# Kernel tuning notes

Hardware: AMD Instinct MI355X
Metric: run time of the kernel (lower is better)

The kernel has to match this reference:

```python
import jax, jax.numpy as jnp
import numpy as np
from jax import lax

N = 256
BATCH = 4096
N_MZIS = N * (N - 1) // 2  # 32640


def _reck_positions(n):
    # Static MZI position schedule: for layer in range(n-1): for pos in range(n-1-layer)
    return np.concatenate([np.arange(n - 1 - layer) for layer in range(n - 1)]).astype(np.int32)


def setup_inputs() -> dict:
    key = jax.random.key(0)
    k1, k2, k3, k4 = jax.random.split(key, 4)
    x = jax.random.normal(k1, (BATCH, N), dtype=jnp.float32)
    theta = jax.random.uniform(k2, (N_MZIS,), dtype=jnp.float32) * (np.pi / 2)
    phi_internal = jax.random.uniform(k3, (N_MZIS,), dtype=jnp.float32) * (2 * np.pi)
    phi_external = jax.random.uniform(k4, (N,), dtype=jnp.float32) * (2 * np.pi)
    return {"x": x, "theta": theta, "phi_internal": phi_internal, "phi_external": phi_external}


def _construct_unitary(theta, phi_internal, phi_external):
    n = phi_external.shape[0]
    positions = jnp.asarray(_reck_positions(n))  # [n_mzis], static schedule

    def step(U, inputs):
        pos, th, ph = inputs
        # Extract the two rows touched by this MZI and apply the 2x2 transfer matrix:
        # [[cos,          -sin*e^{-i phi}],
        #  [sin*e^{i phi}, cos          ]]
        rows = lax.dynamic_slice(U, (pos, jnp.int32(0)), (2, n))  # [2, n]
        r0, r1 = rows[0], rows[1]
        c = jnp.cos(th)
        s = jnp.sin(th)
        e = jnp.cos(ph) + 1j * jnp.sin(ph)
        new_rows = jnp.stack([c * r0 - s * jnp.conj(e) * r1,
                              s * e * r0 + c * r1])
        return lax.dynamic_update_slice(U, new_rows, (pos, jnp.int32(0))), None

    U0 = jnp.eye(n, dtype=jnp.complex64)
    U, _ = lax.scan(step, U0, (positions, theta, phi_internal))
    # Final external phase screen: diag(e^{i phi_ext}) @ U
    phase = jnp.cos(phi_external) + 1j * jnp.sin(phi_external)
    return phase[:, None] * U


def reference(x, theta, phi_internal, phi_external):
    U = _construct_unitary(theta, phi_internal, phi_external)  # [N, N] complex64
    out_c = x.astype(jnp.complex64) @ jnp.conj(U).T            # [B, N] complex64
    return jnp.real(out_c).astype(jnp.float32)
```

## Files before the change

### kernel.cpp

```cpp
#include <hip/hip_runtime.h>


#define NN 256
#define NB 4096

typedef float f32x4 __attribute__((ext_vector_type(4)));
typedef short bf16x8 __attribute__((ext_vector_type(8)));

#define WS_AT_OFF   0u
#define WS_BT_OFF   (512u * 1024u)
#define WS_CF_OFF   (1u << 20)
#define WS_WB_OFF   (2u << 20)

__device__ __forceinline__ unsigned short f2bf(float f) {
    unsigned u = __builtin_bit_cast(unsigned, f);
    unsigned r = (u + 0x7FFFu + ((u >> 16) & 1u)) >> 16;
    return (unsigned short)r;
}

__global__ __launch_bounds__(64) void coeff2_kernel(const float* __restrict__ theta,
                                                    const float* __restrict__ phi,
                                                    f32x4* __restrict__ cf3) {
    const int t = blockIdx.x;
    const int l = threadIdx.x;
    const int g = t >> 3, jj = t & 7;
    const int pA = (t & 1) ? (4 * l + 1) : (4 * l);
#pragma unroll
    for (int s = 0; s < 2; ++s) {
        int p = pA + 2 * s;
        f32x4 v = {1.f, 0.f, 0.f, 0.f};
        if (p <= t && p + t <= 508) {
            int L = (t - p) >> 1;
            int k = ((L * (511 - L)) >> 1) + p;
            float st, ct, sp, cp;
            __sincosf(theta[k], &st, &ct);
            __sincosf(phi[k], &sp, &cp);
            v = (f32x4){ct, st * cp, st * sp, 0.f};
        }
        cf3[(g * 16 + 8 * s + jj) * 64 + l] = v;
    }
}

__device__ __forceinline__ float dpp_up1(float x) {
    int r = __builtin_amdgcn_update_dpp(0, __builtin_bit_cast(int, x), 0x138, 0xF, 0xF, true);
    return __builtin_bit_cast(float, r);
}
__device__ __forceinline__ float dpp_dn1(float x) {
    int r = __builtin_amdgcn_update_dpp(0, __builtin_bit_cast(int, x), 0x130, 0xF, 0xF, true);
    return __builtin_bit_cast(float, r);
}

__device__ __forceinline__ void rot2(float& ar, float& ai, float& br, float& bi, f32x4 co) {
    float c = co.x, sx = co.y, sy = co.z;
    float nar = c * ar - (sx * br + sy * bi);
    float nai = c * ai - (sx * bi - sy * br);
    float nbr = sx * ar - sy * ai + c * br;
    float nbi = sx * ai + sy * ar + c * bi;
    ar = nar; ai = nai; br = nbr; bi = nbi;
}

__device__ __forceinline__ void fence() {
    asm volatile("" ::: "memory");
    __builtin_amdgcn_sched_barrier(0);
}

__global__ __launch_bounds__(64, 1) void build_kernel(const f32x4* __restrict__ cf3,
                                                      float2* __restrict__ Ata,
                                                      float2* __restrict__ Btb) {
    const int l  = threadIdx.x;
    const int r0 = 4 * l;
    const int j  = blockIdx.x;
    const int h  = blockIdx.y;
    const int G0 = 32 * h;
    float2* dst = (h ? Ata : Btb) + (size_t)j * NN;

    float ur0 = (r0 + 0 == j) ? 1.f : 0.f, ui0 = 0.f;
    float ur1 = (r0 + 1 == j) ? 1.f : 0.f, ui1 = 0.f;
    float ur2 = (r0 + 2 == j) ? 1.f : 0.f, ui2 = 0.f;
    float ur3 = (r0 + 3 == j) ? 1.f : 0.f, ui3 = 0.f;
    const float lane0_one = (l == 0) ? 1.f : 0.f;

    f32x4 RA[16], RB[16];

    auto loadgrp = [&](int g, f32x4 (&R)[16]) {
        const f32x4* sp = cf3 + (size_t)g * 1024 + l;
#pragma unroll
        for (int s = 0; s < 16; ++s) R[s] = sp[s * 64];
    };

    auto compute = [&](const f32x4 (&R)[16]) {
#pragma unroll
        for (int jj = 0; jj < 8; ++jj) {
            if ((jj & 1) == 0) {
                rot2(ur0, ui0, ur1, ui1, R[jj]);
                rot2(ur2, ui2, ur3, ui3, R[8 + jj]);
            } else {
                float d0r = dpp_dn1(ur0), d0i = dpp_dn1(ui0);
                float u3r = dpp_up1(ur3), u3i = dpp_up1(ui3);
                f32x4 cb = R[8 + jj];
                float cx = dpp_up1(cb.x) + lane0_one;
                float cy = dpp_up1(cb.y);
                float cz = dpp_up1(cb.z);
                rot2(ur1, ui1, ur2, ui2, R[jj]);
                float n3r = cb.x * ur3 - (cb.y * d0r + cb.z * d0i);
                float n3i = cb.x * ui3 - (cb.y * d0i - cb.z * d0r);
                float n0r = cy * u3r - cz * u3i + cx * ur0;
                float n0i = cy * u3i + cz * u3r + cx * ui0;
                ur3 = n3r; ui3 = n3i; ur0 = n0r; ui0 = n0i;
            }
        }
    };

    loadgrp(G0 + 0, RA);
    fence();
    for (int g = 0; g < 32; g += 2) {
        if (g + 1 < 32) loadgrp(G0 + g + 1, RB);
        fence();
        compute(RA);
        if (g + 2 < 32) loadgrp(G0 + g + 2, RA);
        fence();
        compute(RB);
    }

    *(float4*)(dst + r0)     = make_float4(ur0, ui0, ur1, ui1);
    *(float4*)(dst + r0 + 2) = make_float4(ur2, ui2, ur3, ui3);
}

__global__ __launch_bounds__(256) void mergebf_kernel(const float2* __restrict__ At,
                                                      const float2* __restrict__ Bt,
                                                      const float* __restrict__ phi_ext,
                                                      unsigned short* __restrict__ Wb) {
    __shared__ float2 Ats[64][16];
    __shared__ float2 Bts[16][64];

    const int t  = threadIdx.x;
    const int i0 = blockIdx.x * 16;
    const int j0 = blockIdx.y * 16;
    const int ti = t & 15;
    const int tj = t >> 4;

    float sr = 0.f, si = 0.f;

    for (int kc = 0; kc < NN; kc += 64) {
#pragma unroll
        for (int rep = 0; rep < 2; ++rep) {
            int e = t + rep * 256;
            int k = e >> 3, f = e & 7;
            float4 v = *(const float4*)(At + (size_t)(kc + k) * NN + i0 + 2 * f);
            Ats[k][2 * f]     = make_float2(v.x, v.y);
            Ats[k][2 * f + 1] = make_float2(v.z, v.w);
        }
#pragma unroll
        for (int rep = 0; rep < 2; ++rep) {
            int e = t + rep * 256;
            int j = e >> 5, q = e & 31;
            float4 w = *(const float4*)(Bt + (size_t)(j0 + j) * NN + kc + 2 * q);
            Bts[j][2 * q]     = make_float2(w.x, w.y);
            Bts[j][2 * q + 1] = make_float2(w.z, w.w);
        }
        __syncthreads();
#pragma unroll 8
        for (int k = 0; k < 64; ++k) {
            float2 a = Ats[k][ti];
            float2 b = Bts[tj][k];
            sr += a.x * b.x - a.y * b.y;
            si += a.x * b.y + a.y * b.x;
        }
        __syncthreads();
    }

    float sp, cp;
    __sincosf(phi_ext[i0 + ti], &sp, &cp);
    Wb[(size_t)(i0 + ti) * NN + j0 + tj] = f2bf(cp * sr - sp * si);
}

__global__ __launch_bounds__(256) void gemm_kernel(const float* __restrict__ x,
                                                   const unsigned short* __restrict__ Wb,
                                                   float* __restrict__ out) {
    __shared__ unsigned short Xs[64][72];
    __shared__ unsigned short Ws[64][72];

    const int tid = threadIdx.x;
    const int l   = tid & 63;
    const int wid = tid >> 6;
    const int wm  = wid >> 1, wn = wid & 1;
    const int b0  = blockIdx.x * 64;
    const int i0  = blockIdx.y * 64;

    const int srow = tid >> 2;
    const int sseg = (tid & 3) * 2;

    f32x4 acc[2][2] = {{{0.f, 0.f, 0.f, 0.f}, {0.f, 0.f, 0.f, 0.f}},
                       {{0.f, 0.f, 0.f, 0.f}, {0.f, 0.f, 0.f, 0.f}}};

    const int fr = l & 15;
    const int kg = (l >> 4) * 8;

    for (int k0 = 0; k0 < NN; k0 += 64) {
        const float* xrow = x + (size_t)(b0 + srow) * NN + k0 + sseg * 8;
        float4 a = *(const float4*)(xrow);
        float4 b = *(const float4*)(xrow + 4);
        float4 c = *(const float4*)(xrow + 8);
        float4 d = *(const float4*)(xrow + 12);
        uint4 xv, xv2;
        xv.x  = (unsigned)f2bf(a.x) | ((unsigned)f2bf(a.y) << 16);
        xv.y  = (unsigned)f2bf(a.z) | ((unsigned)f2bf(a.w) << 16);
        xv.z  = (unsigned)f2bf(b.x) | ((unsigned)f2bf(b.y) << 16);
        xv.w  = (unsigned)f2bf(b.z) | ((unsigned)f2bf(b.w) << 16);
        xv2.x = (unsigned)f2bf(c.x) | ((unsigned)f2bf(c.y) << 16);
        xv2.y = (unsigned)f2bf(c.z) | ((unsigned)f2bf(c.w) << 16);
        xv2.z = (unsigned)f2bf(d.x) | ((unsigned)f2bf(d.y) << 16);
        xv2.w = (unsigned)f2bf(d.z) | ((unsigned)f2bf(d.w) << 16);
        uint4 wv  = *(const uint4*)(Wb + (size_t)(i0 + srow) * NN + k0 + sseg * 8);
        uint4 wv2 = *(const uint4*)(Wb + (size_t)(i0 + srow) * NN + k0 + (sseg + 1) * 8);
        *(uint4*)&Xs[srow][sseg * 8]       = xv;
        *(uint4*)&Ws[srow][sseg * 8]       = wv;
        *(uint4*)&Xs[srow][(sseg + 1) * 8] = xv2;
        *(uint4*)&Ws[srow][(sseg + 1) * 8] = wv2;
        __syncthreads();

#pragma unroll
        for (int ks = 0; ks < 2; ++ks) {
            bf16x8 a0  = *(const bf16x8*)&Xs[wm * 32 + fr][ks * 32 + kg];
            bf16x8 a1  = *(const bf16x8*)&Xs[wm * 32 + 16 + fr][ks * 32 + kg];
            bf16x8 bb0 = *(const bf16x8*)&Ws[wn * 32 + fr][ks * 32 + kg];
            bf16x8 bb1 = *(const bf16x8*)&Ws[wn * 32 + 16 + fr][ks * 32 + kg];
            acc[0][0] = __builtin_amdgcn_mfma_f32_16x16x32_bf16(a0, bb0, acc[0][0], 0, 0, 0);
            acc[0][1] = __builtin_amdgcn_mfma_f32_16x16x32_bf16(a0, bb1, acc[0][1], 0, 0, 0);
            acc[1][0] = __builtin_amdgcn_mfma_f32_16x16x32_bf16(a1, bb0, acc[1][0], 0, 0, 0);
            acc[1][1] = __builtin_amdgcn_mfma_f32_16x16x32_bf16(a1, bb1, acc[1][1], 0, 0, 0);
        }
        __syncthreads();
    }

    const int drow = (l >> 4) * 4;
    const int dcol = l & 15;
#pragma unroll
    for (int mf = 0; mf < 2; ++mf)
#pragma unroll
        for (int nf = 0; nf < 2; ++nf) {
            float* op = out + (size_t)(b0 + wm * 32 + mf * 16 + drow) * NN
                      + i0 + wn * 32 + nf * 16 + dcol;
#pragma unroll
            for (int r = 0; r < 4; ++r) op[(size_t)r * NN] = acc[mf][nf][r];
        }
}

extern "C" void kernel_launch(void* const* d_in, const int* in_sizes, int n_in,
                              void* d_out, int out_size, void* d_ws, size_t ws_size,
                              hipStream_t stream) {
    const float* x     = (const float*)d_in[0];
    const float* theta = (const float*)d_in[1];
    const float* phi_i = (const float*)d_in[2];
    const float* phi_e = (const float*)d_in[3];
    float* out = (float*)d_out;

    float2* At  = (float2*)((char*)d_ws + WS_AT_OFF);
    float2* Bt  = (float2*)((char*)d_ws + WS_BT_OFF);
    f32x4*  cf3 = (f32x4*)((char*)d_ws + WS_CF_OFF);
    unsigned short* Wb = (unsigned short*)((char*)d_ws + WS_WB_OFF);

    coeff2_kernel<<<dim3(512), dim3(64), 0, stream>>>(theta, phi_i, cf3);
    build_kernel<<<dim3(256, 2), dim3(64), 0, stream>>>(cf3, At, Bt);
    mergebf_kernel<<<dim3(16, 16), dim3(256), 0, stream>>>(At, Bt, phi_e, Wb);
    gemm_kernel<<<dim3(NB / 64, NN / 64), dim3(256), 0, stream>>>(x, Wb, out);
}
```

Before: 43.75 us.

## Fuse four kernels into one cooperative persistent kernel with grid syncs

Replaces the separate coefficient, build, merge and GEMM launches with a single cooperative kernel of 256 blocks that separates the phases with grid.sync(). Idle warps in the first phase pre-convert x to bf16 in workspace, so the GEMM phase loads bf16 directly. The goal is to remove launch gaps between the small kernels. In exchange, the build phase now uses only 2 of 4 waves per block, and the GEMM phase is limited to 256 blocks with 1 block per CU, which may lower its occupancy compared with the old 256-block launch.

```diff
diff --git a/kernel.cpp b/kernel.cpp
--- a/kernel.cpp
+++ b/kernel.cpp
@@ -1,4 +1,7 @@
 #include <hip/hip_runtime.h>
+#include <hip/hip_cooperative_groups.h>
+
+namespace cg = cooperative_groups;
 
 
 #define NN 256
@@ -7,38 +10,16 @@
 typedef float f32x4 __attribute__((ext_vector_type(4)));
 typedef short bf16x8 __attribute__((ext_vector_type(8)));
 
-#define WS_AT_OFF   0u
-#define WS_BT_OFF   (512u * 1024u)
-#define WS_CF_OFF   (1u << 20)
-#define WS_WB_OFF   (2u << 20)
+#define WS_AT_OFF 0u
+#define WS_BT_OFF (512u * 1024u)
+#define WS_CF_OFF (1u << 20)
+#define WS_WB_OFF (2u << 20)
+#define WS_XB_OFF ((2u << 20) + (256u * 1024u))
 
 __device__ __forceinline__ unsigned short f2bf(float f) {
     unsigned u = __builtin_bit_cast(unsigned, f);
     unsigned r = (u + 0x7FFFu + ((u >> 16) & 1u)) >> 16;
     return (unsigned short)r;
-}
-
-__global__ __launch_bounds__(64) void coeff2_kernel(const float* __restrict__ theta,
-                                                    const float* __restrict__ phi,
-                                                    f32x4* __restrict__ cf3) {
-    const int t = blockIdx.x;
-    const int l = threadIdx.x;
-    const int g = t >> 3, jj = t & 7;
-    const int pA = (t & 1) ? (4 * l + 1) : (4 * l);
-#pragma unroll
-    for (int s = 0; s < 2; ++s) {
-        int p = pA + 2 * s;
-        f32x4 v = {1.f, 0.f, 0.f, 0.f};
-        if (p <= t && p + t <= 508) {
-            int L = (t - p) >> 1;
-            int k = ((L * (511 - L)) >> 1) + p;
-            float st, ct, sp, cp;
-            __sincosf(theta[k], &st, &ct);
-            __sincosf(phi[k], &sp, &cp);
-            v = (f32x4){ct, st * cp, st * sp, 0.f};
-        }
-        cf3[(g * 16 + 8 * s + jj) * 64 + l] = v;
-    }
 }
 
 __device__ __forceinline__ float dpp_up1(float x) {
@@ -64,186 +45,212 @@
     __builtin_amdgcn_sched_barrier(0);
 }
 
-__global__ __launch_bounds__(64, 1) void build_kernel(const f32x4* __restrict__ cf3,
-                                                      float2* __restrict__ Ata,
-                                                      float2* __restrict__ Btb) {
-    const int l  = threadIdx.x;
-    const int r0 = 4 * l;
-    const int j  = blockIdx.x;
-    const int h  = blockIdx.y;
-    const int G0 = 32 * h;
-    float2* dst = (h ? Ata : Btb) + (size_t)j * NN;
-
-    float ur0 = (r0 + 0 == j) ? 1.f : 0.f, ui0 = 0.f;
-    float ur1 = (r0 + 1 == j) ? 1.f : 0.f, ui1 = 0.f;
-    float ur2 = (r0 + 2 == j) ? 1.f : 0.f, ui2 = 0.f;
-    float ur3 = (r0 + 3 == j) ? 1.f : 0.f, ui3 = 0.f;
-    const float lane0_one = (l == 0) ? 1.f : 0.f;
-
-    f32x4 RA[16], RB[16];
-
-    auto loadgrp = [&](int g, f32x4 (&R)[16]) {
-        const f32x4* sp = cf3 + (size_t)g * 1024 + l;
-#pragma unroll
-        for (int s = 0; s < 16; ++s) R[s] = sp[s * 64];
-    };
-
-    auto compute = [&](const f32x4 (&R)[16]) {
-#pragma unroll
-        for (int jj = 0; jj < 8; ++jj) {
-            if ((jj & 1) == 0) {
-                rot2(ur0, ui0, ur1, ui1, R[jj]);
-                rot2(ur2, ui2, ur3, ui3, R[8 + jj]);
-            } else {
-                float d0r = dpp_dn1(ur0), d0i = dpp_dn1(ui0);
-                float u3r = dpp_up1(ur3), u3i = dpp_up1(ui3);
-                f32x4 cb = R[8 + jj];
-                float cx = dpp_up1(cb.x) + lane0_one;
-                float cy = dpp_up1(cb.y);
-                float cz = dpp_up1(cb.z);
-                rot2(ur1, ui1, ur2, ui2, R[jj]);
-                float n3r = cb.x * ur3 - (cb.y * d0r + cb.z * d0i);
-                float n3i = cb.x * ui3 - (cb.y * d0i - cb.z * d0r);
-                float n0r = cy * u3r - cz * u3i + cx * ur0;
-                float n0i = cy * u3i + cz * u3r + cx * ui0;
-                ur3 = n3r; ui3 = n3i; ur0 = n0r; ui0 = n0i;
-            }
-        }
-    };
-
-    loadgrp(G0 + 0, RA);
-    fence();
-    for (int g = 0; g < 32; g += 2) {
-        if (g + 1 < 32) loadgrp(G0 + g + 1, RB);
+__global__ __launch_bounds__(256, 1) void mega_kernel(
+        const float* __restrict__ x, const float* __restrict__ theta,
+        const float* __restrict__ phi_i, const float* __restrict__ phi_e,
+        f32x4* __restrict__ cf3, float2* __restrict__ At, float2* __restrict__ Bt,
+        unsigned short* __restrict__ Wb, unsigned short* __restrict__ xb,
+        float* __restrict__ out) {
+    cg::grid_group grid = cg::this_grid();
+    __shared__ __align__(16) char smem[18432];
+
+    const int bid = blockIdx.x;
+    const int tid = threadIdx.x;
+    const int wid = tid >> 6;
+    const int l   = tid & 63;
+
+    if (wid < 2) {
+        const int t = bid * 2 + wid;
+        const int g = t >> 3, jj = t & 7;
+        const int pA = (t & 1) ? (4 * l + 1) : (4 * l);
+#pragma unroll
+        for (int s = 0; s < 2; ++s) {
+            int p = pA + 2 * s;
+            f32x4 v = {1.f, 0.f, 0.f, 0.f};
+            if (p <= t && p + t <= 508) {
+                int L = (t - p) >> 1;
+                int k = ((L * (511 - L)) >> 1) + p;
+                float st, ct, sp, cp;
+                __sincosf(theta[k], &st, &ct);
+                __sincosf(phi_i[k], &sp, &cp);
+                v = (f32x4){ct, st * cp, st * sp, 0.f};
+            }
+            cf3[(g * 16 + 8 * s + jj) * 64 + l] = v;
+        }
+    } else {
+        const int w2 = bid * 2 + (wid - 2);
+#pragma unroll
+        for (int it = 0; it < 4; ++it) {
+            int gid = w2 * 256 + it * 64 + l;
+            const float4 v0 = ((const float4*)x)[gid * 2];
+            const float4 v1 = ((const float4*)x)[gid * 2 + 1];
+            uint4 w;
+            w.x = (unsigned)f2bf(v0.x) | ((unsigned)f2bf(v0.y) << 16);
+            w.y = (unsigned)f2bf(v0.z) | ((unsigned)f2bf(v0.w) << 16);
+            w.z = (unsigned)f2bf(v1.x) | ((unsigned)f2bf(v1.y) << 16);
+            w.w = (unsigned)f2bf(v1.z) | ((unsigned)f2bf(v1.w) << 16);
+            ((uint4*)xb)[gid] = w;
+        }
+    }
+    grid.sync();
+
+    if (wid < 2) {
+        const int r0 = 4 * l;
+        const int j  = bid;
+        const int h  = wid;
+        const int G0 = 32 * h;
+        float2* dst = (h ? At : Bt) + (size_t)j * NN;
+
+        float ur0 = (r0 + 0 == j) ? 1.f : 0.f, ui0 = 0.f;
+        float ur1 = (r0 + 1 == j) ? 1.f : 0.f, ui1 = 0.f;
+        float ur2 = (r0 + 2 == j) ? 1.f : 0.f, ui2 = 0.f;
+        float ur3 = (r0 + 3 == j) ? 1.f : 0.f, ui3 = 0.f;
+        const float lane0_one = (l == 0) ? 1.f : 0.f;
+
+        f32x4 RA[16], RB[16];
+
+        auto loadgrp = [&](int g, f32x4 (&R)[16]) {
+            const f32x4* sp = cf3 + (size_t)g * 1024 + l;
+#pragma unroll
+            for (int s = 0; s < 16; ++s) R[s] = sp[s * 64];
+        };
+        auto compute = [&](const f32x4 (&R)[16]) {
+#pragma unroll
+            for (int jj = 0; jj < 8; ++jj) {
+                if ((jj & 1) == 0) {
+                    rot2(ur0, ui0, ur1, ui1, R[jj]);
+                    rot2(ur2, ui2, ur3, ui3, R[8 + jj]);
+                } else {
+                    float d0r = dpp_dn1(ur0), d0i = dpp_dn1(ui0);
+                    float u3r = dpp_up1(ur3), u3i = dpp_up1(ui3);
+                    f32x4 cb = R[8 + jj];
+                    float cx = dpp_up1(cb.x) + lane0_one;
+                    float cy = dpp_up1(cb.y);
+                    float cz = dpp_up1(cb.z);
+                    rot2(ur1, ui1, ur2, ui2, R[jj]);
+                    float n3r = cb.x * ur3 - (cb.y * d0r + cb.z * d0i);
+                    float n3i = cb.x * ui3 - (cb.y * d0i - cb.z * d0r);
+                    float n0r = cy * u3r - cz * u3i + cx * ur0;
+                    float n0i = cy * u3i + cz * u3r + cx * ui0;
+                    ur3 = n3r; ui3 = n3i; ur0 = n0r; ui0 = n0i;
+                }
+            }
+        };
+
+        loadgrp(G0 + 0, RA);
         fence();
-        compute(RA);
-        if (g + 2 < 32) loadgrp(G0 + g + 2, RA);
-        fence();
-        compute(RB);
-    }
-
-    *(float4*)(dst + r0)     = make_float4(ur0, ui0, ur1, ui1);
-    *(float4*)(dst + r0 + 2) = make_float4(ur2, ui2, ur3, ui3);
-}
-
-__global__ __launch_bounds__(256) void mergebf_kernel(const float2* __restrict__ At,
-                                                      const float2* __restrict__ Bt,
-                                                      const float* __restrict__ phi_ext,
-                                                      unsigned short* __restrict__ Wb) {
-    __shared__ float2 Ats[64][16];
-    __shared__ float2 Bts[16][64];
-
-    const int t  = threadIdx.x;
-    const int i0 = blockIdx.x * 16;
-    const int j0 = blockIdx.y * 16;
-    const int ti = t & 15;
-    const int tj = t >> 4;
-
-    float sr = 0.f, si = 0.f;
-
-    for (int kc = 0; kc < NN; kc += 64) {
-#pragma unroll
-        for (int rep = 0; rep < 2; ++rep) {
-            int e = t + rep * 256;
-            int k = e >> 3, f = e & 7;
-            float4 v = *(const float4*)(At + (size_t)(kc + k) * NN + i0 + 2 * f);
-            Ats[k][2 * f]     = make_float2(v.x, v.y);
-            Ats[k][2 * f + 1] = make_float2(v.z, v.w);
-        }
-#pragma unroll
-        for (int rep = 0; rep < 2; ++rep) {
-            int e = t + rep * 256;
-            int j = e >> 5, q = e & 31;
-            float4 w = *(const float4*)(Bt + (size_t)(j0 + j) * NN + kc + 2 * q);
-            Bts[j][2 * q]     = make_float2(w.x, w.y);
-            Bts[j][2 * q + 1] = make_float2(w.z, w.w);
-        }
-        __syncthreads();
+        for (int g = 0; g < 32; g += 2) {
+            if (g + 1 < 32) loadgrp(G0 + g + 1, RB);
+            fence();
+            compute(RA);
+            if (g + 2 < 32) loadgrp(G0 + g + 2, RA);
+            fence();
+            compute(RB);
+        }
+
+        *(float4*)(dst + r0)     = make_float4(ur0, ui0, ur1, ui1);
+        *(float4*)(dst + r0 + 2) = make_float4(ur2, ui2, ur3, ui3);
+    }
+    grid.sync();
+
+    {
+        float2* Ats = (float2*)smem;
+        float2* Bts = (float2*)(smem + 8192);
+        const int i0 = (bid & 15) * 16;
+        const int j0 = (bid >> 4) * 16;
+        const int ti = tid & 15;
+        const int tj = tid >> 4;
+
+        float sr = 0.f, si = 0.f;
+
+        for (int kc = 0; kc < NN; kc += 64) {
+#pragma unroll
+            for (int rep = 0; rep < 2; ++rep) {
+                int e = tid + rep * 256;
+                int k = e >> 3, f = e & 7;
+                float4 v = *(const float4*)(At + (size_t)(kc + k) * NN + i0 + 2 * f);
+                Ats[k * 16 + 2 * f]     = make_float2(v.x, v.y);
+                Ats[k * 16 + 2 * f + 1] = make_float2(v.z, v.w);
+            }
+#pragma unroll
+            for (int rep = 0; rep < 2; ++rep) {
+                int e = tid + rep * 256;
+                int j = e >> 5, q = e & 31;
+                float4 w = *(const float4*)(Bt + (size_t)(j0 + j) * NN + kc + 2 * q);
+                Bts[j * 64 + 2 * q]     = make_float2(w.x, w.y);
+                Bts[j * 64 + 2 * q + 1] = make_float2(w.z, w.w);
+            }
+            __syncthreads();
 #pragma unroll 8
-        for (int k = 0; k < 64; ++k) {
-            float2 a = Ats[k][ti];
-            float2 b = Bts[tj][k];
-            sr += a.x * b.x - a.y * b.y;
-            si += a.x * b.y + a.y * b.x;
-        }
-        __syncthreads();
-    }
-
-    float sp, cp;
-    __sincosf(phi_ext[i0 + ti], &sp, &cp);
-    Wb[(size_t)(i0 + ti) * NN + j0 + tj] = f2bf(cp * sr - sp * si);
-}
-
-__global__ __launch_bounds__(256) void gemm_kernel(const float* __restrict__ x,
-                                                   const unsigned short* __restrict__ Wb,
-                                                   float* __restrict__ out) {
-    __shared__ unsigned short Xs[64][72];
-    __shared__ unsigned short Ws[64][72];
-
-    const int tid = threadIdx.x;
-    const int l   = tid & 63;
-    const int wid = tid >> 6;
-    const int wm  = wid >> 1, wn = wid & 1;
-    const int b0  = blockIdx.x * 64;
-    const int i0  = blockIdx.y * 64;
-
-    const int srow = tid >> 2;
-    const int sseg = (tid & 3) * 2;
-
-    f32x4 acc[2][2] = {{{0.f, 0.f, 0.f, 0.f}, {0.f, 0.f, 0.f, 0.f}},
-                       {{0.f, 0.f, 0.f, 0.f}, {0.f, 0.f, 0.f, 0.f}}};
-
-    const int fr = l & 15;
-    const int kg = (l >> 4) * 8;
-
-    for (int k0 = 0; k0 < NN; k0 += 64) {
-        const float* xrow = x + (size_t)(b0 + srow) * NN + k0 + sseg * 8;
-        float4 a = *(const float4*)(xrow);
-        float4 b = *(const float4*)(xrow + 4);
-        float4 c = *(const float4*)(xrow + 8);
-        float4 d = *(const float4*)(xrow + 12);
-        uint4 xv, xv2;
-        xv.x  = (unsigned)f2bf(a.x) | ((unsigned)f2bf(a.y) << 16);
-        xv.y  = (unsigned)f2bf(a.z) | ((unsigned)f2bf(a.w) << 16);
-        xv.z  = (unsigned)f2bf(b.x) | ((unsigned)f2bf(b.y) << 16);
-        xv.w  = (unsigned)f2bf(b.z) | ((unsigned)f2bf(b.w) << 16);
-        xv2.x = (unsigned)f2bf(c.x) | ((unsigned)f2bf(c.y) << 16);
-        xv2.y = (unsigned)f2bf(c.z) | ((unsigned)f2bf(c.w) << 16);
-        xv2.z = (unsigned)f2bf(d.x) | ((unsigned)f2bf(d.y) << 16);
-        xv2.w = (unsigned)f2bf(d.z) | ((unsigned)f2bf(d.w) << 16);
-        uint4 wv  = *(const uint4*)(Wb + (size_t)(i0 + srow) * NN + k0 + sseg * 8);
-        uint4 wv2 = *(const uint4*)(Wb + (size_t)(i0 + srow) * NN + k0 + (sseg + 1) * 8);
-        *(uint4*)&Xs[srow][sseg * 8]       = xv;
-        *(uint4*)&Ws[srow][sseg * 8]       = wv;
-        *(uint4*)&Xs[srow][(sseg + 1) * 8] = xv2;
-        *(uint4*)&Ws[srow][(sseg + 1) * 8] = wv2;
-        __syncthreads();
-
-#pragma unroll
-        for (int ks = 0; ks < 2; ++ks) {
-            bf16x8 a0  = *(const bf16x8*)&Xs[wm * 32 + fr][ks * 32 + kg];
-            bf16x8 a1  = *(const bf16x8*)&Xs[wm * 32 + 16 + fr][ks * 32 + kg];
-            bf16x8 bb0 = *(const bf16x8*)&Ws[wn * 32 + fr][ks * 32 + kg];
-            bf16x8 bb1 = *(const bf16x8*)&Ws[wn * 32 + 16 + fr][ks * 32 + kg];
-            acc[0][0] = __builtin_amdgcn_mfma_f32_16x16x32_bf16(a0, bb0, acc[0][0], 0, 0, 0);
-            acc[0][1] = __builtin_amdgcn_mfma_f32_16x16x32_bf16(a0, bb1, acc[0][1], 0, 0, 0);
-            acc[1][0] = __builtin_amdgcn_mfma_f32_16x16x32_bf16(a1, bb0, acc[1][0], 0, 0, 0);
-            acc[1][1] = __builtin_amdgcn_mfma_f32_16x16x32_bf16(a1, bb1, acc[1][1], 0, 0, 0);
-        }
-        __syncthreads();
-    }
-
-    const int drow = (l >> 4) * 4;
-    const int dcol = l & 15;
-#pragma unroll
-    for (int mf = 0; mf < 2; ++mf)
-#pragma unroll
-        for (int nf = 0; nf < 2; ++nf) {
-            float* op = out + (size_t)(b0 + wm * 32 + mf * 16 + drow) * NN
-                      + i0 + wn * 32 + nf * 16 + dcol;
-#pragma unroll
-            for (int r = 0; r < 4; ++r) op[(size_t)r * NN] = acc[mf][nf][r];
-        }
+            for (int k = 0; k < 64; ++k) {
+                float2 a = Ats[k * 16 + ti];
+                float2 b = Bts[tj * 64 + k];
+                sr += a.x * b.x - a.y * b.y;
+                si += a.x * b.y + a.y * b.x;
+            }
+            __syncthreads();
+        }
+
+        float sp, cp;
+        __sincosf(phi_e[i0 + ti], &sp, &cp);
+        Wb[(size_t)(i0 + ti) * NN + j0 + tj] = f2bf(cp * sr - sp * si);
+    }
+    grid.sync();
+
+    {
+        unsigned short (*Xs)[72] = (unsigned short (*)[72])smem;
+        unsigned short (*Ws)[72] = (unsigned short (*)[72])(smem + 9216);
+
+        const int wm = wid >> 1, wn = wid & 1;
+        const int b0 = (bid >> 2) * 64;
+        const int i0 = (bid & 3) * 64;
+
+        const int srow = tid >> 2;
+        const int sseg = (tid & 3) * 2;
+
+        f32x4 acc[2][2] = {{{0.f, 0.f, 0.f, 0.f}, {0.f, 0.f, 0.f, 0.f}},
+                           {{0.f, 0.f, 0.f, 0.f}, {0.f, 0.f, 0.f, 0.f}}};
+
+        const int fr = l & 15;
+        const int kg = (l >> 4) * 8;
+
+        for (int k0 = 0; k0 < NN; k0 += 64) {
+            uint4 xv  = *(const uint4*)(xb + (size_t)(b0 + srow) * NN + k0 + sseg * 8);
+            uint4 wv  = *(const uint4*)(Wb + (size_t)(i0 + srow) * NN + k0 + sseg * 8);
+            uint4 xv2 = *(const uint4*)(xb + (size_t)(b0 + srow) * NN + k0 + (sseg + 1) * 8);
+            uint4 wv2 = *(const uint4*)(Wb + (size_t)(i0 + srow) * NN + k0 + (sseg + 1) * 8);
+            *(uint4*)&Xs[srow][sseg * 8]       = xv;
+            *(uint4*)&Ws[srow][sseg * 8]       = wv;
+            *(uint4*)&Xs[srow][(sseg + 1) * 8] = xv2;
+            *(uint4*)&Ws[srow][(sseg + 1) * 8] = wv2;
+            __syncthreads();
+
+#pragma unroll
+            for (int ks = 0; ks < 2; ++ks) {
+                bf16x8 a0  = *(const bf16x8*)&Xs[wm * 32 + fr][ks * 32 + kg];
+                bf16x8 a1  = *(const bf16x8*)&Xs[wm * 32 + 16 + fr][ks * 32 + kg];
+                bf16x8 bb0 = *(const bf16x8*)&Ws[wn * 32 + fr][ks * 32 + kg];
+                bf16x8 bb1 = *(const bf16x8*)&Ws[wn * 32 + 16 + fr][ks * 32 + kg];
+                acc[0][0] = __builtin_amdgcn_mfma_f32_16x16x32_bf16(a0, bb0, acc[0][0], 0, 0, 0);
+                acc[0][1] = __builtin_amdgcn_mfma_f32_16x16x32_bf16(a0, bb1, acc[0][1], 0, 0, 0);
+                acc[1][0] = __builtin_amdgcn_mfma_f32_16x16x32_bf16(a1, bb0, acc[1][0], 0, 0, 0);
+                acc[1][1] = __builtin_amdgcn_mfma_f32_16x16x32_bf16(a1, bb1, acc[1][1], 0, 0, 0);
+            }
+            __syncthreads();
+        }
+
+        const int drow = (l >> 4) * 4;
+        const int dcol = l & 15;
+#pragma unroll
+        for (int mf = 0; mf < 2; ++mf)
+#pragma unroll
+            for (int nf = 0; nf < 2; ++nf) {
+                float* op = out + (size_t)(b0 + wm * 32 + mf * 16 + drow) * NN
+                          + i0 + wn * 32 + nf * 16 + dcol;
+#pragma unroll
+                for (int r = 0; r < 4; ++r) op[(size_t)r * NN] = acc[mf][nf][r];
+            }
+    }
 }
 
 extern "C" void kernel_launch(void* const* d_in, const int* in_sizes, int n_in,
@@ -255,13 +262,15 @@
     const float* phi_e = (const float*)d_in[3];
     float* out = (float*)d_out;
 
+    f32x4*  cf3 = (f32x4*)((char*)d_ws + WS_CF_OFF);
     float2* At  = (float2*)((char*)d_ws + WS_AT_OFF);
     float2* Bt  = (float2*)((char*)d_ws + WS_BT_OFF);
-    f32x4*  cf3 = (f32x4*)((char*)d_ws + WS_CF_OFF);
     unsigned short* Wb = (unsigned short*)((char*)d_ws + WS_WB_OFF);
-
-    coeff2_kernel<<<dim3(512), dim3(64), 0, stream>>>(theta, phi_i, cf3);
-    build_kernel<<<dim3(256, 2), dim3(64), 0, stream>>>(cf3, At, Bt);
-    mergebf_kernel<<<dim3(16, 16), dim3(256), 0, stream>>>(At, Bt, phi_e, Wb);
-    gemm_kernel<<<dim3(NB / 64, NN / 64), dim3(256), 0, stream>>>(x, Wb, out);
-}
+    unsigned short* xb = (unsigned short*)((char*)d_ws + WS_XB_OFF);
+
+    void* args[] = {(void*)&x, (void*)&theta, (void*)&phi_i, (void*)&phi_e,
+                    (void*)&cf3, (void*)&At, (void*)&Bt, (void*)&Wb, (void*)&xb,
+                    (void*)&out};
+    hipLaunchCooperativeKernel((const void*)mega_kernel, dim3(256), dim3(256),
+                               args, 0, stream);
+}
```

After: 153.0 us. +249.7%, slower.
